# Kernel optimization log

Measured on AMD Instinct MI355X. Metric: run time of the kernel, lower is better.

Reference implementation:

```python
import jax, jax.numpy as jnp
import numpy as np
from jax import lax

B, N, C_FEAT = 16, 32768, 128
NPOINT = 2048
BIG = 1e10  # initial 'infinite' distance, matches torch's 1e10


def farthest_point_sample(xyz, npoint):
    """xyz: [B,N,3] -> indices [B,npoint] via iterative FPS.
    Deterministic start at index 0 (original uses a random start index)."""
    b, n, c = xyz.shape

    def step(carry, _):
        distance, farthest = carry                      # [B,N], [B]
        centroid = jnp.take_along_axis(
            xyz, farthest[:, None, None], axis=1)       # [B,1,3]
        dist = jnp.sum((xyz - centroid) ** 2, axis=-1)  # [B,N]
        distance = jnp.minimum(distance, dist)          # running min dist to chosen set
        new_farthest = jnp.argmax(distance, axis=-1)    # [B]
        return (distance, new_farthest), farthest

    init = (jnp.full((b, n), BIG, xyz.dtype), jnp.zeros((b,), jnp.int32))
    _, idxs = lax.scan(step, init, None, length=npoint)  # [npoint, B]
    return idxs.T                                        # [B, npoint]


def index_points(points, idx):
    """points: [B,N,D], idx: [B,S] -> [B,S,D] gather."""
    return jnp.take_along_axis(points, idx[:, :, None], axis=1)


def setup_inputs() -> dict:
    key = jax.random.key(0)
    k1, k2 = jax.random.split(key)
    xyz = jax.random.normal(k1, (B, N, 3), dtype=jnp.float32)
    features = jax.random.normal(k2, (B, N, C_FEAT), dtype=jnp.float32)
    return {"xyz": xyz, "features": features, "npoint": NPOINT}


def reference(xyz, features, npoint):
    fps_idx = farthest_point_sample(xyz, npoint)   # [B,npoint]
    new_xyz = index_points(xyz, fps_idx)           # [B,npoint,3]
    new_features = index_points(features, fps_idx) # [B,npoint,C]
    return (new_xyz, new_features)
```

## Files before the change

### kernel.cpp

```cpp
#include <hip/hip_runtime.h>

#define BATCH   16
#define NPTS    32768
#define NPOINT  2048
#define C_FEAT  128
#define NSEG    512
#define NTH     1024
#define NW      16


__device__ __forceinline__ unsigned part4(unsigned v) {
  return (v & 1u) | ((v & 2u) << 2) | ((v & 4u) << 4) | ((v & 8u) << 6);
}
__device__ __forceinline__ int morton(float x, float y, float z) {
  const unsigned qx = (unsigned)min(15, max(0, (int)((x + 4.0f) * 2.0f)));
  const unsigned qy = (unsigned)min(15, max(0, (int)((y + 4.0f) * 2.0f)));
  const unsigned qz = (unsigned)min(15, max(0, (int)((z + 4.0f) * 2.0f)));
  return (int)(part4(qx) | (part4(qy) << 1) | (part4(qz) << 2));
}

__device__ __forceinline__ unsigned long long u64max(unsigned long long a,
                                                     unsigned long long b) {
  return a > b ? a : b;
}
__device__ __forceinline__ unsigned long long shflxor_u64(
    unsigned long long v, int off) {
  const unsigned lo = (unsigned)v, hi = (unsigned)(v >> 32);
  const unsigned olo = (unsigned)__shfl_xor((int)lo, off);
  const unsigned ohi = (unsigned)__shfl_xor((int)hi, off);
  return ((unsigned long long)ohi << 32) | olo;
}

__global__ __launch_bounds__(NTH) void sort_kernel(
    const float* __restrict__ xyz, float4* __restrict__ pts) {
  const int b = blockIdx.x, t = threadIdx.x, lane = t & 63;
  const float* __restrict__ base = xyz + (size_t)b * NPTS * 3;
  __shared__ unsigned bins[4096];
  __shared__ unsigned wsum[NW];

  for (int i = t; i < 4096; i += NTH) bins[i] = 0u;
  __syncthreads();
  for (int k = 0; k < 32; ++k) {
    const int p = k * NTH + t;
    atomicAdd(&bins[morton(base[p*3], base[p*3+1], base[p*3+2])], 1u);
  }
  __syncthreads();

  unsigned c0 = bins[4*t], c1 = bins[4*t+1], c2 = bins[4*t+2], c3 = bins[4*t+3];
  const unsigned mysum = c0 + c1 + c2 + c3;
  unsigned acc = mysum;
#pragma unroll
  for (int d = 1; d < 64; d <<= 1) {
    unsigned n = __shfl_up(acc, d);
    if (lane >= d) acc += n;
  }
  if (lane == 63) wsum[t >> 6] = acc;
  __syncthreads();
  unsigned woff = 0;
  for (int w = 0; w < (t >> 6); ++w) woff += wsum[w];
  unsigned run = woff + acc - mysum;
  bins[4*t]   = run; run += c0;
  bins[4*t+1] = run; run += c1;
  bins[4*t+2] = run; run += c2;
  bins[4*t+3] = run;
  __syncthreads();

  float4* __restrict__ pb = pts + (size_t)b * NPTS;
  for (int k = 0; k < 32; ++k) {
    const int p = k * NTH + t;
    const float x = base[p*3], y = base[p*3+1], z = base[p*3+2];
    const unsigned pos = atomicAdd(&bins[morton(x, y, z)], 1u);
    pb[pos] = make_float4(x, y, z, __int_as_float(p));
  }
}

__global__ __launch_bounds__(NTH) void fps_kernel(
    const float4* __restrict__ pts_g, int* __restrict__ fps_idx) {
  const int b = blockIdx.x, t = threadIdx.x, lane = t & 63, w = t >> 6;
  const float4* __restrict__ P = pts_g + (size_t)b * NPTS;

  __shared__ float              dmin[NPTS];
  __shared__ float              sb[6][NSEG];
  __shared__ float              cand[3][NSEG];
  __shared__ unsigned long long pack[NSEG];
  __shared__ unsigned long long s_red[2][8];
  __shared__ unsigned short     wl[NSEG];
  __shared__ int                s_cnt[2];

  for (int r = 0; r < 32; ++r) {
    const int seg = w * 32 + r;
    const int i = seg * 64 + lane;
    const float4 q = P[i];
    dmin[i] = 1e10f;
    const unsigned mykey = ((unsigned)__float_as_int(q.w) << 15) | (unsigned)i;
    float xl = q.x, xh = q.x, yl = q.y, yh = q.y, zl = q.z, zh = q.z;
    unsigned k = mykey;
#pragma unroll
    for (int off = 32; off > 0; off >>= 1) {
      xl = fminf(xl, __shfl_xor(xl, off)); xh = fmaxf(xh, __shfl_xor(xh, off));
      yl = fminf(yl, __shfl_xor(yl, off)); yh = fmaxf(yh, __shfl_xor(yh, off));
      zl = fminf(zl, __shfl_xor(zl, off)); zh = fmaxf(zh, __shfl_xor(zh, off));
      k  = min(k, (unsigned)__shfl_xor((int)k, off));
    }
    if (lane == 0) {
      sb[0][seg] = xl; sb[1][seg] = xh;
      sb[2][seg] = yl; sb[3][seg] = yh;
      sb[4][seg] = zl; sb[5][seg] = zh;
      pack[seg] = ((unsigned long long)__float_as_uint(1e10f) << 32) |
                  (unsigned long long)(0x3FFFFFFFu - k);
    }
    if (mykey == k) {
      cand[0][seg] = q.x; cand[1][seg] = q.y; cand[2][seg] = q.z;
    }
  }
  if (t == 0) { s_cnt[0] = 0; s_cnt[1] = 0; }
  __syncthreads();

  if (t < NSEG) {
    unsigned long long p = pack[t];
#pragma unroll
    for (int off = 32; off > 0; off >>= 1) p = u64max(p, shflxor_u64(p, off));
    if (lane == 0) s_red[0][w] = p;
  }
  __syncthreads();

  for (int s = 0; s < NPOINT; ++s) {
    unsigned long long p = s_red[s & 1][0];
#pragma unroll
    for (int j = 1; j < 8; ++j) p = u64max(p, s_red[s & 1][j]);
    const unsigned kwin = 0x3FFFFFFFu - (unsigned)(p & 0x3FFFFFFFu);
    const int far  = (int)(kwin >> 15);
    const int segw = (int)((kwin & 0x7FFFu) >> 6);
    const float cx = cand[0][segw], cy = cand[1][segw], cz = cand[2][segw];

    if (t == 0) fps_idx[b * NPOINT + s] = far;
    if (t == NTH - 1) s_cnt[(s + 1) & 1] = 0;

    if (t < NSEG) {
      const unsigned long long pk = pack[t];
      const float cm = __uint_as_float((unsigned)(pk >> 32));
      const float ddx = fmaxf(fmaxf(sb[0][t] - cx, cx - sb[1][t]), 0.0f);
      const float ddy = fmaxf(fmaxf(sb[2][t] - cy, cy - sb[3][t]), 0.0f);
      const float ddz = fmaxf(fmaxf(sb[4][t] - cz, cz - sb[5][t]), 0.0f);
      const float r2 = ddx * ddx + ddy * ddy + ddz * ddz;
      const bool need = !(r2 * 0.999f > cm);
      const unsigned long long bal = __ballot(need);
      int wb = 0;
      if (lane == 0 && bal != 0ull)
        wb = atomicAdd(&s_cnt[s & 1], (int)__popcll(bal));
      wb = __shfl(wb, 0);
      if (need) {
        const unsigned long long ltm = (1ull << lane) - 1ull;
        wl[wb + (int)__popcll(bal & ltm)] = (unsigned short)t;
      }
    }
    __syncthreads();

    const int C = s_cnt[s & 1];
    int e = w;
    for (; e + NW < C; e += 2 * NW) {
      const int segA = (int)wl[e], segB = (int)wl[e + NW];
      const int iA = segA * 64 + lane, iB = segB * 64 + lane;
      const float4 qA = P[iA];
      const float4 qB = P[iB];
      const float dmA = dmin[iA], dmB = dmin[iB];
      const float dxA = qA.x - cx, dyA = qA.y - cy, dzA = qA.z - cz;
      const float dxB = qB.x - cx, dyB = qB.y - cy, dzB = qB.z - cz;
      const float dA = __builtin_fmaf(dzA, dzA, __builtin_fmaf(dyA, dyA, dxA*dxA));
      const float dB = __builtin_fmaf(dzB, dzB, __builtin_fmaf(dyB, dyB, dxB*dxB));
      const float ndA = fminf(dmA, dA), ndB = fminf(dmB, dB);
      dmin[iA] = ndA; dmin[iB] = ndB;
      const unsigned kA = ((unsigned)__float_as_int(qA.w) << 15) | (unsigned)iA;
      const unsigned kB = ((unsigned)__float_as_int(qB.w) << 15) | (unsigned)iB;
      unsigned long long pA = ((unsigned long long)__float_as_uint(ndA) << 32) |
                              (unsigned long long)(0x3FFFFFFFu - kA);
      unsigned long long pB = ((unsigned long long)__float_as_uint(ndB) << 32) |
                              (unsigned long long)(0x3FFFFFFFu - kB);
      const unsigned long long pA0 = pA, pB0 = pB;
#pragma unroll
      for (int off = 32; off > 0; off >>= 1) {
        pA = u64max(pA, shflxor_u64(pA, off));
        pB = u64max(pB, shflxor_u64(pB, off));
      }
      if (lane == 0) { pack[segA] = pA; pack[segB] = pB; }
      if (pA0 == pA) { cand[0][segA] = qA.x; cand[1][segA] = qA.y; cand[2][segA] = qA.z; }
      if (pB0 == pB) { cand[0][segB] = qB.x; cand[1][segB] = qB.y; cand[2][segB] = qB.z; }
    }
    for (; e < C; e += NW) {
      const int seg = (int)wl[e];
      const int i = seg * 64 + lane;
      const float4 q = P[i];
      const float dx = q.x - cx, dy = q.y - cy, dz = q.z - cz;
      const float d = __builtin_fmaf(dz, dz, __builtin_fmaf(dy, dy, dx * dx));
      const float nd = fminf(dmin[i], d);
      dmin[i] = nd;
      const unsigned k = ((unsigned)__float_as_int(q.w) << 15) | (unsigned)i;
      unsigned long long pk = ((unsigned long long)__float_as_uint(nd) << 32) |
                              (unsigned long long)(0x3FFFFFFFu - k);
      const unsigned long long pk0 = pk;
#pragma unroll
      for (int off = 32; off > 0; off >>= 1) pk = u64max(pk, shflxor_u64(pk, off));
      if (lane == 0) pack[seg] = pk;
      if (pk0 == pk) { cand[0][seg] = q.x; cand[1][seg] = q.y; cand[2][seg] = q.z; }
    }
    __syncthreads();

    if (t < NSEG) {
      unsigned long long pk = pack[t];
#pragma unroll
      for (int off = 32; off > 0; off >>= 1) pk = u64max(pk, shflxor_u64(pk, off));
      if (lane == 0) s_red[(s + 1) & 1][w] = pk;
    }
    __syncthreads();
  }
}

__global__ __launch_bounds__(256) void gather_kernel(
    const float* __restrict__ xyz, const float* __restrict__ feat,
    const int* __restrict__ fps_idx, float* __restrict__ out) {
  const int lane = threadIdx.x & 31;
  const int sub  = threadIdx.x >> 5;
  const int row  = blockIdx.x * 8 + sub;
  const int b    = row >> 11;
  const int src  = fps_idx[row];

  const float4* __restrict__ f =
      reinterpret_cast<const float4*>(feat + ((size_t)b * NPTS + src) * C_FEAT);
  float4* __restrict__ o =
      reinterpret_cast<float4*>(out + (size_t)BATCH * NPOINT * 3 +
                                (size_t)row * C_FEAT);
  o[lane] = f[lane];
  if (lane < 3) {
    out[(size_t)row * 3 + lane] = xyz[((size_t)b * NPTS + src) * 3 + lane];
  }
}

extern "C" void kernel_launch(void* const* d_in, const int* in_sizes, int n_in,
                              void* d_out, int out_size, void* d_ws, size_t ws_size,
                              hipStream_t stream) {
  (void)in_sizes; (void)n_in; (void)out_size; (void)ws_size;
  const float* xyz  = (const float*)d_in[0];
  const float* feat = (const float*)d_in[1];
  float* out = (float*)d_out;

  char* ws = (char*)d_ws;
  int*    fps_idx = (int*)ws;
  float4* pts     = (float4*)(ws + (1u << 20));

  sort_kernel<<<BATCH, NTH, 0, stream>>>(xyz, pts);
  fps_kernel<<<BATCH, NTH, 0, stream>>>(pts, fps_idx);
  gather_kernel<<<(BATCH * NPOINT) / 8, 256, 0, stream>>>(xyz, feat, fps_idx, out);
}
```

Before: 4.372 ms.

## Use 32-point segments with center/extent bounds and fetch winner from global

Halves the segment size from 64 to 32 points (1024 segments) so the bounding-box pruning test is finer and fewer points are recomputed per FPS step. Segment bounds are stored as a center plus conservatively rounded-up bf16 extents to save shared memory. The per-segment candidate coordinate cache is removed: the winning point is re-read from global memory by its sorted index. This adds a dependent global load on every step's critical path, and half-wave reductions now run over 32-lane groups.

```diff
diff --git a/kernel.cpp b/kernel.cpp
--- a/kernel.cpp
+++ b/kernel.cpp
@@ -4,7 +4,7 @@
 #define NPTS    32768
 #define NPOINT  2048
 #define C_FEAT  128
-#define NSEG    512
+#define NSEG    1024
 #define NTH     1024
 #define NW      16
 
@@ -29,6 +29,12 @@
   const unsigned olo = (unsigned)__shfl_xor((int)lo, off);
   const unsigned ohi = (unsigned)__shfl_xor((int)hi, off);
   return ((unsigned long long)ohi << 32) | olo;
+}
+__device__ __forceinline__ unsigned short bfup(float e) {
+  const unsigned u = __float_as_uint(e);
+  unsigned short b = (unsigned short)(u >> 16);
+  if (__uint_as_float(((unsigned)b) << 16) < e) ++b;
+  return b;
 }
 
 __global__ __launch_bounds__(NTH) void sort_kernel(
@@ -77,47 +83,52 @@
 __global__ __launch_bounds__(NTH) void fps_kernel(
     const float4* __restrict__ pts_g, int* __restrict__ fps_idx) {
   const int b = blockIdx.x, t = threadIdx.x, lane = t & 63, w = t >> 6;
+  const int hw = t >> 5, hl = t & 31;
   const float4* __restrict__ P = pts_g + (size_t)b * NPTS;
 
   __shared__ float              dmin[NPTS];
-  __shared__ float              sb[6][NSEG];
-  __shared__ float              cand[3][NSEG];
   __shared__ unsigned long long pack[NSEG];
+  __shared__ float              cenx[NSEG], ceny[NSEG], cenz[NSEG];
+  __shared__ unsigned short     extx[NSEG], exty[NSEG], extz[NSEG];
   __shared__ unsigned long long s_red[2][8];
   __shared__ unsigned short     wl[NSEG];
   __shared__ int                s_cnt[2];
 
   for (int r = 0; r < 32; ++r) {
-    const int seg = w * 32 + r;
-    const int i = seg * 64 + lane;
+    const int seg = r * 32 + hw;
+    const int i = seg * 32 + hl;
     const float4 q = P[i];
     dmin[i] = 1e10f;
-    const unsigned mykey = ((unsigned)__float_as_int(q.w) << 15) | (unsigned)i;
     float xl = q.x, xh = q.x, yl = q.y, yh = q.y, zl = q.z, zh = q.z;
-    unsigned k = mykey;
-#pragma unroll
-    for (int off = 32; off > 0; off >>= 1) {
+    unsigned k = ((unsigned)__float_as_int(q.w) << 15) | (unsigned)i;
+#pragma unroll
+    for (int off = 16; off > 0; off >>= 1) {
       xl = fminf(xl, __shfl_xor(xl, off)); xh = fmaxf(xh, __shfl_xor(xh, off));
       yl = fminf(yl, __shfl_xor(yl, off)); yh = fmaxf(yh, __shfl_xor(yh, off));
       zl = fminf(zl, __shfl_xor(zl, off)); zh = fmaxf(zh, __shfl_xor(zh, off));
       k  = min(k, (unsigned)__shfl_xor((int)k, off));
     }
-    if (lane == 0) {
-      sb[0][seg] = xl; sb[1][seg] = xh;
-      sb[2][seg] = yl; sb[3][seg] = yh;
-      sb[4][seg] = zl; sb[5][seg] = zh;
+    if (hl == 0) {
+      const float cxm = 0.5f * (xl + xh);
+      const float cym = 0.5f * (yl + yh);
+      const float czm = 0.5f * (zl + zh);
+      float ex = fmaxf(xh - cxm, cxm - xl);
+      float ey = fmaxf(yh - cym, cym - yl);
+      float ez = fmaxf(zh - czm, czm - zl);
+      ex = __uint_as_float(__float_as_uint(ex) + 2);
+      ey = __uint_as_float(__float_as_uint(ey) + 2);
+      ez = __uint_as_float(__float_as_uint(ez) + 2);
+      cenx[seg] = cxm; ceny[seg] = cym; cenz[seg] = czm;
+      extx[seg] = bfup(ex); exty[seg] = bfup(ey); extz[seg] = bfup(ez);
       pack[seg] = ((unsigned long long)__float_as_uint(1e10f) << 32) |
                   (unsigned long long)(0x3FFFFFFFu - k);
     }
-    if (mykey == k) {
-      cand[0][seg] = q.x; cand[1][seg] = q.y; cand[2][seg] = q.z;
-    }
   }
   if (t == 0) { s_cnt[0] = 0; s_cnt[1] = 0; }
   __syncthreads();
 
-  if (t < NSEG) {
-    unsigned long long p = pack[t];
+  if (t < 512) {
+    unsigned long long p = u64max(pack[t], pack[t + 512]);
 #pragma unroll
     for (int off = 32; off > 0; off >>= 1) p = u64max(p, shflxor_u64(p, off));
     if (lane == 0) s_red[0][w] = p;
@@ -129,19 +140,22 @@
 #pragma unroll
     for (int j = 1; j < 8; ++j) p = u64max(p, s_red[s & 1][j]);
     const unsigned kwin = 0x3FFFFFFFu - (unsigned)(p & 0x3FFFFFFFu);
-    const int far  = (int)(kwin >> 15);
-    const int segw = (int)((kwin & 0x7FFFu) >> 6);
-    const float cx = cand[0][segw], cy = cand[1][segw], cz = cand[2][segw];
+    const int far = (int)(kwin >> 15);
+    const float4 qn = P[(int)(kwin & 0x7FFFu)];
+    const float cx = qn.x, cy = qn.y, cz = qn.z;
 
     if (t == 0) fps_idx[b * NPOINT + s] = far;
     if (t == NTH - 1) s_cnt[(s + 1) & 1] = 0;
 
-    if (t < NSEG) {
+    {
       const unsigned long long pk = pack[t];
       const float cm = __uint_as_float((unsigned)(pk >> 32));
-      const float ddx = fmaxf(fmaxf(sb[0][t] - cx, cx - sb[1][t]), 0.0f);
-      const float ddy = fmaxf(fmaxf(sb[2][t] - cy, cy - sb[3][t]), 0.0f);
-      const float ddz = fmaxf(fmaxf(sb[4][t] - cz, cz - sb[5][t]), 0.0f);
+      const float ex = __uint_as_float(((unsigned)extx[t]) << 16);
+      const float ey = __uint_as_float(((unsigned)exty[t]) << 16);
+      const float ez = __uint_as_float(((unsigned)extz[t]) << 16);
+      const float ddx = fmaxf(fabsf(cx - cenx[t]) - ex, 0.0f);
+      const float ddy = fmaxf(fabsf(cy - ceny[t]) - ey, 0.0f);
+      const float ddz = fmaxf(fabsf(cz - cenz[t]) - ez, 0.0f);
       const float r2 = ddx * ddx + ddy * ddy + ddz * ddz;
       const bool need = !(r2 * 0.999f > cm);
       const unsigned long long bal = __ballot(need);
@@ -157,10 +171,10 @@
     __syncthreads();
 
     const int C = s_cnt[s & 1];
-    int e = w;
-    for (; e + NW < C; e += 2 * NW) {
-      const int segA = (int)wl[e], segB = (int)wl[e + NW];
-      const int iA = segA * 64 + lane, iB = segB * 64 + lane;
+    int e = hw;
+    for (; e + 32 < C; e += 64) {
+      const int segA = (int)wl[e], segB = (int)wl[e + 32];
+      const int iA = segA * 32 + hl, iB = segB * 32 + hl;
       const float4 qA = P[iA];
       const float4 qB = P[iB];
       const float dmA = dmin[iA], dmB = dmin[iB];
@@ -176,19 +190,16 @@
                               (unsigned long long)(0x3FFFFFFFu - kA);
       unsigned long long pB = ((unsigned long long)__float_as_uint(ndB) << 32) |
                               (unsigned long long)(0x3FFFFFFFu - kB);
-      const unsigned long long pA0 = pA, pB0 = pB;
-#pragma unroll
-      for (int off = 32; off > 0; off >>= 1) {
+#pragma unroll
+      for (int off = 16; off > 0; off >>= 1) {
         pA = u64max(pA, shflxor_u64(pA, off));
         pB = u64max(pB, shflxor_u64(pB, off));
       }
-      if (lane == 0) { pack[segA] = pA; pack[segB] = pB; }
-      if (pA0 == pA) { cand[0][segA] = qA.x; cand[1][segA] = qA.y; cand[2][segA] = qA.z; }
-      if (pB0 == pB) { cand[0][segB] = qB.x; cand[1][segB] = qB.y; cand[2][segB] = qB.z; }
-    }
-    for (; e < C; e += NW) {
+      if (hl == 0) { pack[segA] = pA; pack[segB] = pB; }
+    }
+    for (; e < C; e += 32) {
       const int seg = (int)wl[e];
-      const int i = seg * 64 + lane;
+      const int i = seg * 32 + hl;
       const float4 q = P[i];
       const float dx = q.x - cx, dy = q.y - cy, dz = q.z - cz;
       const float d = __builtin_fmaf(dz, dz, __builtin_fmaf(dy, dy, dx * dx));
@@ -197,16 +208,14 @@
       const unsigned k = ((unsigned)__float_as_int(q.w) << 15) | (unsigned)i;
       unsigned long long pk = ((unsigned long long)__float_as_uint(nd) << 32) |
                               (unsigned long long)(0x3FFFFFFFu - k);
-      const unsigned long long pk0 = pk;
-#pragma unroll
-      for (int off = 32; off > 0; off >>= 1) pk = u64max(pk, shflxor_u64(pk, off));
-      if (lane == 0) pack[seg] = pk;
-      if (pk0 == pk) { cand[0][seg] = q.x; cand[1][seg] = q.y; cand[2][seg] = q.z; }
+#pragma unroll
+      for (int off = 16; off > 0; off >>= 1) pk = u64max(pk, shflxor_u64(pk, off));
+      if (hl == 0) pack[seg] = pk;
     }
     __syncthreads();
 
-    if (t < NSEG) {
-      unsigned long long pk = pack[t];
+    if (t < 512) {
+      unsigned long long pk = u64max(pack[t], pack[t + 512]);
 #pragma unroll
       for (int off = 32; off > 0; off >>= 1) pk = u64max(pk, shflxor_u64(pk, off));
       if (lane == 0) s_red[(s + 1) & 1][w] = pk;
```

Result: faster. 3.829 ms, median of 2 (-12.4%).
